# Optimization experiments

Measured on AMD Instinct MI355X. Metric: run time of the kernel, lower is better.

Reference implementation:

```python
import jax, jax.numpy as jnp
import numpy as np

N_USERS = 50000
N_ENTITIES = 250000
N_RELATIONS = 24
EMBED_DIM = 128
RELATION_DIM = 128
KG_BATCH = 16384
KG_L2_LAMBDA = 1e-5


def _l2_loss_mean(x):
    # mean over batch of (||x||^2 / 2)
    return jnp.mean(jnp.sum(x * x, axis=1) / 2.0)


def setup_inputs() -> dict:
    key = jax.random.key(0)
    k1, k2, k3, k4, k5, k6, k7 = jax.random.split(key, 7)
    n_total = N_ENTITIES + N_USERS
    # xavier-uniform-like init scale
    s_e = float(np.sqrt(6.0 / (n_total + EMBED_DIM)))
    s_r = float(np.sqrt(6.0 / (N_RELATIONS + RELATION_DIM)))
    s_m = float(np.sqrt(6.0 / (EMBED_DIM + RELATION_DIM)))
    entity_user_embed = jax.random.uniform(k1, (n_total, EMBED_DIM), jnp.float32, -s_e, s_e)
    relation_embed = jax.random.uniform(k2, (N_RELATIONS, RELATION_DIM), jnp.float32, -s_r, s_r)
    trans_M = jax.random.uniform(k3, (N_RELATIONS, EMBED_DIM, RELATION_DIM), jnp.float32, -s_m, s_m)
    h = jax.random.randint(k4, (KG_BATCH,), 0, n_total, dtype=jnp.int64 if jax.config.jax_enable_x64 else jnp.int32)
    r = jax.random.randint(k5, (KG_BATCH,), 0, N_RELATIONS, dtype=h.dtype)
    pos_t = jax.random.randint(k6, (KG_BATCH,), 0, n_total, dtype=h.dtype)
    neg_t = jax.random.randint(k7, (KG_BATCH,), 0, n_total, dtype=h.dtype)
    return {
        "entity_user_embed": entity_user_embed,
        "relation_embed": relation_embed,
        "trans_M": trans_M,
        "h": h,
        "r": r,
        "pos_t": pos_t,
        "neg_t": neg_t,
    }


def reference(entity_user_embed, relation_embed, trans_M, h, r, pos_t, neg_t):
    # KGAT.calc_kg_loss (mode='train_kg')
    r_embed = relation_embed[r]            # [B, R]
    W_r = trans_M[r]                       # [B, E, R] per-edge TransR matrix (gather)
    h_embed = entity_user_embed[h]         # [B, E]
    pos_t_embed = entity_user_embed[pos_t] # [B, E]
    neg_t_embed = entity_user_embed[neg_t] # [B, E]

    # bmm([B,1,E], [B,E,R]) -> [B,R]
    r_mul_h = jnp.einsum('be,ber->br', h_embed, W_r)
    r_mul_pos_t = jnp.einsum('be,ber->br', pos_t_embed, W_r)
    r_mul_neg_t = jnp.einsum('be,ber->br', neg_t_embed, W_r)

    pos_score = jnp.sum(jnp.square(r_mul_h + r_embed - r_mul_pos_t), axis=1)
    neg_score = jnp.sum(jnp.square(r_mul_h + r_embed - r_mul_neg_t), axis=1)

    kg_loss = jnp.mean(-jax.nn.log_sigmoid(neg_score - pos_score))
    l2_loss = (_l2_loss_mean(r_mul_h) + _l2_loss_mean(r_embed)
               + _l2_loss_mean(r_mul_pos_t) + _l2_loss_mean(r_mul_neg_t))
    return kg_loss + KG_L2_LAMBDA * l2_loss
```

## Files before the change

kernel.cpp:

```cpp
#include <hip/hip_runtime.h>
#include <math.h>

#define KG_B    16384
#define KG_D    128
#define KG_NR   24
#define KG_TM   32
#define KG_BPAD (KG_B + KG_NR * KG_TM)
#define KG_NGRP (KG_BPAD / KG_TM)

#define WS_BSUM KG_BPAD
#define WS_PREW_BYTES 131072

typedef __attribute__((ext_vector_type(8))) short bf16x8;
typedef __attribute__((ext_vector_type(4))) float f32x4;

__device__ __forceinline__ unsigned bf16r(float f) {
    return (__float_as_uint(f) + 0x8000u) >> 16;
}
__device__ __forceinline__ unsigned pack2(float lo, float hi) {
    return bf16r(lo) | (bf16r(hi) << 16);
}

__global__ __launch_bounds__(1024) void kg_sort_prep(const int* __restrict__ r,
                                                     const float* __restrict__ M,
                                                     int* __restrict__ perm,
                                                     unsigned short* __restrict__ preW) {
    __shared__ int cntw[16][25];
    __shared__ int basew[16][25];
    __shared__ int pbase_s[24];
    __shared__ int cnt_tot[24];
    __shared__ int total_s;
    __shared__ __align__(16) unsigned short sWp[KG_D * KG_D];

    const int t = threadIdx.x;

    if (blockIdx.x != 0) {
        const int k  = blockIdx.x - 1;
        const int e  = t >> 3;
        const int c0 = (t & 7) * 16;
        const float* src = M + ((size_t)k << 14) + (size_t)e * KG_D + c0;
        float4 rw[4];
#pragma unroll
        for (int f = 0; f < 4; ++f) rw[f] = ((const float4*)src)[f];
#pragma unroll
        for (int dc = 0; dc < 16; ++dc) {
            const int col = c0 + dc;
            const float v = ((const float*)&rw[0])[dc];
            sWp[col * KG_D + (e ^ ((col & 7) << 3))] = (unsigned short)bf16r(v);
        }
        __syncthreads();
        uint4* dst = (uint4*)(preW + ((size_t)k << 14));
        const uint4* s4 = (const uint4*)sWp;
        dst[2 * t]     = s4[2 * t];
        dst[2 * t + 1] = s4[2 * t + 1];
        return;
    }

    const int w = t >> 6;
    int* cz = &cntw[0][0];
    for (int i = t; i < 16 * 25; i += 1024) cz[i] = 0;
    __syncthreads();

    int kt[16];
#pragma unroll
    for (int j = 0; j < 16; ++j) kt[j] = r[j * 1024 + t];
#pragma unroll
    for (int j = 0; j < 16; ++j) atomicAdd(&cntw[w][kt[j]], 1);
    __syncthreads();

    if (t < 24) {
        int s = 0;
        for (int w2 = 0; w2 < 16; ++w2) { basew[w2][t] = s; s += cntw[w2][t]; }
        cnt_tot[t] = s;
    }
    __syncthreads();
    if (t == 0) {
        int run = 0;
        for (int k = 0; k < 24; ++k) {
            pbase_s[k] = run;
            run += (cnt_tot[k] + (KG_TM - 1)) & ~(KG_TM - 1);
        }
        total_s = run;
    }
    __syncthreads();
    if (t < 24)
        for (int w2 = 0; w2 < 16; ++w2) basew[w2][t] += pbase_s[t];
    for (int i = t; i < 16 * 25; i += 1024) cz[i] = 0;
    __syncthreads();

#pragma unroll
    for (int j = 0; j < 16; ++j) {
        const int k = kt[j];
        const int pos = basew[w][k] + atomicAdd(&cntw[w][k], 1);
        perm[pos] = j * 1024 + t;
    }
    __syncthreads();

    if (t < 24) {
        const int e0 = pbase_s[t] + cnt_tot[t];
        const int e1 = pbase_s[t] + ((cnt_tot[t] + (KG_TM - 1)) & ~(KG_TM - 1));
        for (int p = e0; p < e1; ++p) perm[p] = -1;
    }
    for (int i = total_s + t; i < KG_BPAD; i += 1024) perm[i] = -1;
}

__global__ __launch_bounds__(256, 2) void kg_main(
    const float* __restrict__ ent, const float* __restrict__ rel,
    const unsigned short* __restrict__ preW,
    const int* __restrict__ h,     const int* __restrict__ r,
    const int* __restrict__ pt,    const int* __restrict__ nt,
    const int* __restrict__ perm,  float* __restrict__ bsum)
{
    __shared__ __align__(16) unsigned short sX[3 * KG_TM * KG_D];
    __shared__ __align__(16) unsigned short sW[KG_D * KG_D];
    __shared__ float sScr[2][KG_TM][4];

    const int tid   = threadIdx.x;
    const int slot0 = blockIdx.x * KG_TM;
    const int p0    = perm[slot0];
    if (p0 < 0) {
        if (tid == 0) bsum[blockIdx.x] = 0.f;
        return;
    }
    const int rb = __builtin_amdgcn_readfirstlane(r[p0]);

    {
        const char* gsrc = (const char*)(preW + ((size_t)rb << 14));
        char* ldsb = (char*)&sW[0];
        const int w4   = tid >> 6;
        const int lane = tid & 63;
#pragma unroll
        for (int q = 0; q < 8; ++q) {
            const int off = q * 4096 + w4 * 1024;
            __builtin_amdgcn_global_load_lds(
                (const unsigned int*)(gsrc + off + lane * 16),
                (unsigned int*)(ldsb + off), 16, 0, 0);
        }
    }

    {
        const int g  = tid >> 3;
        const int e0 = (tid & 7) * 16;
        const int pg = perm[slot0 + g];
        const int bb = pg < 0 ? p0 : pg;
        const int idx3[3] = { h[bb], pt[bb], nt[bb] };
        const int sw = (g & 7) << 3;
#pragma unroll
        for (int t3 = 0; t3 < 3; ++t3) {
            const float* src = ent + (size_t)idx3[t3] * KG_D + e0;
            const float4 f0 = ((const float4*)src)[0];
            const float4 f1 = ((const float4*)src)[1];
            const float4 f2 = ((const float4*)src)[2];
            const float4 f3 = ((const float4*)src)[3];
            uint4 u0, u1;
            u0.x = pack2(f0.x, f0.y); u0.y = pack2(f0.z, f0.w);
            u0.z = pack2(f1.x, f1.y); u0.w = pack2(f1.z, f1.w);
            u1.x = pack2(f2.x, f2.y); u1.y = pack2(f2.z, f2.w);
            u1.z = pack2(f3.x, f3.y); u1.w = pack2(f3.z, f3.w);
            unsigned short* base = sX + t3 * (KG_TM * KG_D) + g * KG_D;
            *(uint4*)(base + ((e0    ) ^ sw)) = u0;
            *(uint4*)(base + ((e0 + 8) ^ sw)) = u1;
        }
    }
    __syncthreads();

    const int l   = tid & 63;
    const int w   = tid >> 6;
    const int rt  = w & 1;
    const int chs = w >> 1;
    const int li  = l & 15;
    const int kq  = l >> 4;

    const int ar  = rt * 16 + li;
    const int asw = (ar & 7) << 3;

    f32x4 acc[3][4];
#pragma unroll
    for (int t3 = 0; t3 < 3; ++t3)
#pragma unroll
        for (int n = 0; n < 4; ++n) acc[t3][n] = (f32x4)0.f;

#pragma unroll
    for (int kk = 0; kk < 4; ++kk) {
        const int e0 = kk * 32 + kq * 8;
        bf16x8 af[3];
#pragma unroll
        for (int t3 = 0; t3 < 3; ++t3)
            af[t3] = *(const bf16x8*)&sX[t3 * (KG_TM * KG_D) + ar * KG_D + (e0 ^ asw)];
#pragma unroll
        for (int n = 0; n < 4; ++n) {
            const int col = chs * 64 + n * 16 + li;
            const bf16x8 bfr = *(const bf16x8*)&sW[col * KG_D + (e0 ^ ((col & 7) << 3))];
            acc[0][n] = __builtin_amdgcn_mfma_f32_16x16x32_bf16(af[0], bfr, acc[0][n], 0, 0, 0);
            acc[1][n] = __builtin_amdgcn_mfma_f32_16x16x32_bf16(af[1], bfr, acc[1][n], 0, 0, 0);
            acc[2][n] = __builtin_amdgcn_mfma_f32_16x16x32_bf16(af[2], bfr, acc[2][n], 0, 0, 0);
        }
    }

    float ps[4] = {0,0,0,0}, ns[4] = {0,0,0,0}, sq[4] = {0,0,0,0};
    const float* relrow = rel + (size_t)rb * KG_D + chs * 64;
#pragma unroll
    for (int n = 0; n < 4; ++n) {
        const float rv = relrow[n * 16 + li];
#pragma unroll
        for (int j = 0; j < 4; ++j) {
            const float va = acc[0][n][j];
            const float vp = acc[1][n][j];
            const float vn = acc[2][n][j];
            const float s  = va + rv;
            const float dp = s - vp;
            const float dn = s - vn;
            ps[j] += dp * dp;
            ns[j] += dn * dn;
            sq[j] += va * va + vp * vp + vn * vn + rv * rv;
        }
    }
#pragma unroll
    for (int j = 0; j < 4; ++j)
#pragma unroll
        for (int m = 1; m < 16; m <<= 1) {
            ps[j] += __shfl_xor(ps[j], m);
            ns[j] += __shfl_xor(ns[j], m);
            sq[j] += __shfl_xor(sq[j], m);
        }

    if (li == 0) {
#pragma unroll
        for (int j = 0; j < 4; ++j) {
            const int row = rt * 16 + kq * 4 + j;
            sScr[chs][row][0] = ps[j];
            sScr[chs][row][1] = ns[j];
            sScr[chs][row][2] = sq[j];
        }
    }
    __syncthreads();

    if (tid < 64) {
        float term = 0.f;
        if (tid < KG_TM) {
            const int row = tid;
            const float P = sScr[0][row][0] + sScr[1][row][0];
            const float N = sScr[0][row][1] + sScr[1][row][1];
            const float S = sScr[0][row][2] + sScr[1][row][2];
            const int pg = perm[slot0 + row];
            if (pg >= 0) {
                const float x = P - N;
                term = fmaxf(x, 0.f) + log1pf(expf(-fabsf(x)))
                     + 5e-6f * S;
            }
        }
#pragma unroll
        for (int off = 16; off > 0; off >>= 1) term += __shfl_down(term, off);
        if (tid == 0) bsum[blockIdx.x] = term;
    }
}

__global__ __launch_bounds__(256) void kg_final(const float* __restrict__ bsum,
                                                float* __restrict__ out) {
    __shared__ float s[256];
    const int t = threadIdx.x;
    float acc = 0.f;
    for (int i = t; i < KG_NGRP; i += 256) acc += bsum[i];
    s[t] = acc;
    __syncthreads();
    for (int off = 128; off > 0; off >>= 1) {
        if (t < off) s[t] += s[t + off];
        __syncthreads();
    }
    if (t == 0) out[0] = s[0] * (1.0f / (float)KG_B);
}

extern "C" void kernel_launch(void* const* d_in, const int* in_sizes, int n_in,
                              void* d_out, int out_size, void* d_ws, size_t ws_size,
                              hipStream_t stream) {
    const float* ent = (const float*)d_in[0];
    const float* rel = (const float*)d_in[1];
    const float* M   = (const float*)d_in[2];
    const int*   h   = (const int*)d_in[3];
    const int*   r   = (const int*)d_in[4];
    const int*   pt  = (const int*)d_in[5];
    const int*   nt  = (const int*)d_in[6];

    int*            perm = (int*)d_ws;
    float*          bsum = (float*)d_ws + WS_BSUM;
    unsigned short* preW = (unsigned short*)((char*)d_ws + WS_PREW_BYTES);
    float*          out  = (float*)d_out;

    kg_sort_prep<<<1 + KG_NR, 1024, 0, stream>>>(r, M, perm, preW);
    kg_main     <<<KG_NGRP, 256, 0, stream>>>(ent, rel, preW, h, r, pt, nt, perm, bsum);
    kg_final    <<<1, 256, 0, stream>>>(bsum, out);
}
```

Baseline: 27.89 us.

## Load A-fragments directly to registers and fuse final reduction via atomics

Removes the shared-memory staging of gathered entity rows: each lane now loads and converts its MFMA A-fragments straight from global memory into registers. This frees LDS, so launch bounds are raised to 3 blocks per CU. It also drops the separate final-reduction kernel. Each block instead adds its partial sum into a fixed-point 64-bit global accumulator, and the last block to finish writes the result. The trade-offs are uncoalesced-ish per-lane gathers, global atomic contention, and fixed-point quantization of the sum.

```diff
diff --git a/kernel.cpp b/kernel.cpp
--- a/kernel.cpp
+++ b/kernel.cpp
@@ -8,8 +8,10 @@
 #define KG_BPAD (KG_B + KG_NR * KG_TM)
 #define KG_NGRP (KG_BPAD / KG_TM)
 
-#define WS_BSUM KG_BPAD
+#define WS_ACC_BYTES  68608
+#define WS_DONE_BYTES 68616
 #define WS_PREW_BYTES 131072
+#define KG_SCALE      1099511627776.0
 
 typedef __attribute__((ext_vector_type(8))) short bf16x8;
 typedef __attribute__((ext_vector_type(4))) float f32x4;
@@ -24,6 +26,8 @@
 __global__ __launch_bounds__(1024) void kg_sort_prep(const int* __restrict__ r,
                                                      const float* __restrict__ M,
                                                      int* __restrict__ perm,
+                                                     unsigned long long* __restrict__ acc,
+                                                     unsigned int* __restrict__ done,
                                                      unsigned short* __restrict__ preW) {
     __shared__ int cntw[16][25];
     __shared__ int basew[16][25];
@@ -56,6 +60,8 @@
         return;
     }
 
+    if (t == 0) { *acc = 0ull; *done = 0u; }
+
     const int w = t >> 6;
     int* cz = &cntw[0][0];
     for (int i = t; i < 16 * 25; i += 1024) cz[i] = 0;
@@ -104,170 +110,156 @@
     for (int i = total_s + t; i < KG_BPAD; i += 1024) perm[i] = -1;
 }
 
-__global__ __launch_bounds__(256, 2) void kg_main(
+__global__ __launch_bounds__(256, 3) void kg_main(
     const float* __restrict__ ent, const float* __restrict__ rel,
     const unsigned short* __restrict__ preW,
     const int* __restrict__ h,     const int* __restrict__ r,
     const int* __restrict__ pt,    const int* __restrict__ nt,
-    const int* __restrict__ perm,  float* __restrict__ bsum)
+    const int* __restrict__ perm,
+    unsigned long long* __restrict__ acc,
+    unsigned int* __restrict__ done,
+    float* __restrict__ out)
 {
-    __shared__ __align__(16) unsigned short sX[3 * KG_TM * KG_D];
     __shared__ __align__(16) unsigned short sW[KG_D * KG_D];
     __shared__ float sScr[2][KG_TM][4];
 
     const int tid   = threadIdx.x;
     const int slot0 = blockIdx.x * KG_TM;
     const int p0    = perm[slot0];
-    if (p0 < 0) {
-        if (tid == 0) bsum[blockIdx.x] = 0.f;
-        return;
-    }
-    const int rb = __builtin_amdgcn_readfirstlane(r[p0]);
-
-    {
-        const char* gsrc = (const char*)(preW + ((size_t)rb << 14));
-        char* ldsb = (char*)&sW[0];
-        const int w4   = tid >> 6;
-        const int lane = tid & 63;
-#pragma unroll
-        for (int q = 0; q < 8; ++q) {
-            const int off = q * 4096 + w4 * 1024;
-            __builtin_amdgcn_global_load_lds(
-                (const unsigned int*)(gsrc + off + lane * 16),
-                (unsigned int*)(ldsb + off), 16, 0, 0);
-        }
-    }
-
-    {
-        const int g  = tid >> 3;
-        const int e0 = (tid & 7) * 16;
-        const int pg = perm[slot0 + g];
-        const int bb = pg < 0 ? p0 : pg;
+
+    float bs = 0.f;
+
+    if (p0 >= 0) {
+        const int rb = __builtin_amdgcn_readfirstlane(r[p0]);
+
+        {
+            const char* gsrc = (const char*)(preW + ((size_t)rb << 14));
+            char* ldsb = (char*)&sW[0];
+            const int w4   = tid >> 6;
+            const int lane = tid & 63;
+#pragma unroll
+            for (int q = 0; q < 8; ++q) {
+                const int off = q * 4096 + w4 * 1024;
+                __builtin_amdgcn_global_load_lds(
+                    (const unsigned int*)(gsrc + off + lane * 16),
+                    (unsigned int*)(ldsb + off), 16, 0, 0);
+            }
+        }
+
+        const int l   = tid & 63;
+        const int w   = tid >> 6;
+        const int rt  = w & 1;
+        const int chs = w >> 1;
+        const int li  = l & 15;
+        const int kq  = l >> 4;
+
+        const int ar = rt * 16 + li;
+        const int pr = perm[slot0 + ar];
+        const int bb = pr < 0 ? p0 : pr;
         const int idx3[3] = { h[bb], pt[bb], nt[bb] };
-        const int sw = (g & 7) << 3;
+        bf16x8 af[3][4];
 #pragma unroll
         for (int t3 = 0; t3 < 3; ++t3) {
-            const float* src = ent + (size_t)idx3[t3] * KG_D + e0;
-            const float4 f0 = ((const float4*)src)[0];
-            const float4 f1 = ((const float4*)src)[1];
-            const float4 f2 = ((const float4*)src)[2];
-            const float4 f3 = ((const float4*)src)[3];
-            uint4 u0, u1;
-            u0.x = pack2(f0.x, f0.y); u0.y = pack2(f0.z, f0.w);
-            u0.z = pack2(f1.x, f1.y); u0.w = pack2(f1.z, f1.w);
-            u1.x = pack2(f2.x, f2.y); u1.y = pack2(f2.z, f2.w);
-            u1.z = pack2(f3.x, f3.y); u1.w = pack2(f3.z, f3.w);
-            unsigned short* base = sX + t3 * (KG_TM * KG_D) + g * KG_D;
-            *(uint4*)(base + ((e0    ) ^ sw)) = u0;
-            *(uint4*)(base + ((e0 + 8) ^ sw)) = u1;
-        }
-    }
-    __syncthreads();
-
-    const int l   = tid & 63;
-    const int w   = tid >> 6;
-    const int rt  = w & 1;
-    const int chs = w >> 1;
-    const int li  = l & 15;
-    const int kq  = l >> 4;
-
-    const int ar  = rt * 16 + li;
-    const int asw = (ar & 7) << 3;
-
-    f32x4 acc[3][4];
-#pragma unroll
-    for (int t3 = 0; t3 < 3; ++t3)
-#pragma unroll
-        for (int n = 0; n < 4; ++n) acc[t3][n] = (f32x4)0.f;
-
-#pragma unroll
-    for (int kk = 0; kk < 4; ++kk) {
-        const int e0 = kk * 32 + kq * 8;
-        bf16x8 af[3];
+            const float* xb = ent + (size_t)idx3[t3] * KG_D;
+#pragma unroll
+            for (int kk = 0; kk < 4; ++kk) {
+                const int e0 = kk * 32 + kq * 8;
+                const float4 a0 = *(const float4*)(xb + e0);
+                const float4 a1 = *(const float4*)(xb + e0 + 4);
+                union { uint4 u; bf16x8 v; } cv;
+                cv.u.x = pack2(a0.x, a0.y); cv.u.y = pack2(a0.z, a0.w);
+                cv.u.z = pack2(a1.x, a1.y); cv.u.w = pack2(a1.z, a1.w);
+                af[t3][kk] = cv.v;
+            }
+        }
+        __syncthreads();
+
+        f32x4 accf[3][4];
 #pragma unroll
         for (int t3 = 0; t3 < 3; ++t3)
-            af[t3] = *(const bf16x8*)&sX[t3 * (KG_TM * KG_D) + ar * KG_D + (e0 ^ asw)];
+#pragma unroll
+            for (int n = 0; n < 4; ++n) accf[t3][n] = (f32x4)0.f;
+
+#pragma unroll
+        for (int kk = 0; kk < 4; ++kk) {
+            const int e0 = kk * 32 + kq * 8;
+#pragma unroll
+            for (int n = 0; n < 4; ++n) {
+                const int col = chs * 64 + n * 16 + li;
+                const bf16x8 bfr = *(const bf16x8*)&sW[col * KG_D + (e0 ^ ((col & 7) << 3))];
+                accf[0][n] = __builtin_amdgcn_mfma_f32_16x16x32_bf16(af[0][kk], bfr, accf[0][n], 0, 0, 0);
+                accf[1][n] = __builtin_amdgcn_mfma_f32_16x16x32_bf16(af[1][kk], bfr, accf[1][n], 0, 0, 0);
+                accf[2][n] = __builtin_amdgcn_mfma_f32_16x16x32_bf16(af[2][kk], bfr, accf[2][n], 0, 0, 0);
+            }
+        }
+
+        float ps[4] = {0,0,0,0}, ns[4] = {0,0,0,0}, sq[4] = {0,0,0,0};
+        const float* relrow = rel + (size_t)rb * KG_D + chs * 64;
 #pragma unroll
         for (int n = 0; n < 4; ++n) {
-            const int col = chs * 64 + n * 16 + li;
-            const bf16x8 bfr = *(const bf16x8*)&sW[col * KG_D + (e0 ^ ((col & 7) << 3))];
-            acc[0][n] = __builtin_amdgcn_mfma_f32_16x16x32_bf16(af[0], bfr, acc[0][n], 0, 0, 0);
-            acc[1][n] = __builtin_amdgcn_mfma_f32_16x16x32_bf16(af[1], bfr, acc[1][n], 0, 0, 0);
-            acc[2][n] = __builtin_amdgcn_mfma_f32_16x16x32_bf16(af[2], bfr, acc[2][n], 0, 0, 0);
-        }
-    }
-
-    float ps[4] = {0,0,0,0}, ns[4] = {0,0,0,0}, sq[4] = {0,0,0,0};
-    const float* relrow = rel + (size_t)rb * KG_D + chs * 64;
-#pragma unroll
-    for (int n = 0; n < 4; ++n) {
-        const float rv = relrow[n * 16 + li];
-#pragma unroll
-        for (int j = 0; j < 4; ++j) {
-            const float va = acc[0][n][j];
-            const float vp = acc[1][n][j];
-            const float vn = acc[2][n][j];
-            const float s  = va + rv;
-            const float dp = s - vp;
-            const float dn = s - vn;
-            ps[j] += dp * dp;
-            ns[j] += dn * dn;
-            sq[j] += va * va + vp * vp + vn * vn + rv * rv;
-        }
-    }
-#pragma unroll
-    for (int j = 0; j < 4; ++j)
-#pragma unroll
-        for (int m = 1; m < 16; m <<= 1) {
-            ps[j] += __shfl_xor(ps[j], m);
-            ns[j] += __shfl_xor(ns[j], m);
-            sq[j] += __shfl_xor(sq[j], m);
-        }
-
-    if (li == 0) {
-#pragma unroll
-        for (int j = 0; j < 4; ++j) {
-            const int row = rt * 16 + kq * 4 + j;
-            sScr[chs][row][0] = ps[j];
-            sScr[chs][row][1] = ns[j];
-            sScr[chs][row][2] = sq[j];
-        }
-    }
-    __syncthreads();
-
-    if (tid < 64) {
-        float term = 0.f;
-        if (tid < KG_TM) {
-            const int row = tid;
-            const float P = sScr[0][row][0] + sScr[1][row][0];
-            const float N = sScr[0][row][1] + sScr[1][row][1];
-            const float S = sScr[0][row][2] + sScr[1][row][2];
-            const int pg = perm[slot0 + row];
-            if (pg >= 0) {
-                const float x = P - N;
-                term = fmaxf(x, 0.f) + log1pf(expf(-fabsf(x)))
-                     + 5e-6f * S;
-            }
-        }
-#pragma unroll
-        for (int off = 16; off > 0; off >>= 1) term += __shfl_down(term, off);
-        if (tid == 0) bsum[blockIdx.x] = term;
-    }
-}
-
-__global__ __launch_bounds__(256) void kg_final(const float* __restrict__ bsum,
-                                                float* __restrict__ out) {
-    __shared__ float s[256];
-    const int t = threadIdx.x;
-    float acc = 0.f;
-    for (int i = t; i < KG_NGRP; i += 256) acc += bsum[i];
-    s[t] = acc;
-    __syncthreads();
-    for (int off = 128; off > 0; off >>= 1) {
-        if (t < off) s[t] += s[t + off];
+            const float rv = relrow[n * 16 + li];
+#pragma unroll
+            for (int j = 0; j < 4; ++j) {
+                const float va = accf[0][n][j];
+                const float vp = accf[1][n][j];
+                const float vn = accf[2][n][j];
+                const float s  = va + rv;
+                const float dp = s - vp;
+                const float dn = s - vn;
+                ps[j] += dp * dp;
+                ns[j] += dn * dn;
+                sq[j] += va * va + vp * vp + vn * vn + rv * rv;
+            }
+        }
+#pragma unroll
+        for (int j = 0; j < 4; ++j)
+#pragma unroll
+            for (int m = 1; m < 16; m <<= 1) {
+                ps[j] += __shfl_xor(ps[j], m);
+                ns[j] += __shfl_xor(ns[j], m);
+                sq[j] += __shfl_xor(sq[j], m);
+            }
+
+        if (li == 0) {
+#pragma unroll
+            for (int j = 0; j < 4; ++j) {
+                const int row = rt * 16 + kq * 4 + j;
+                sScr[chs][row][0] = ps[j];
+                sScr[chs][row][1] = ns[j];
+                sScr[chs][row][2] = sq[j];
+            }
+        }
         __syncthreads();
-    }
-    if (t == 0) out[0] = s[0] * (1.0f / (float)KG_B);
+
+        if (tid < 64) {
+            float term = 0.f;
+            if (tid < KG_TM) {
+                const int row = tid;
+                const float P = sScr[0][row][0] + sScr[1][row][0];
+                const float N = sScr[0][row][1] + sScr[1][row][1];
+                const float S = sScr[0][row][2] + sScr[1][row][2];
+                const int pg = perm[slot0 + row];
+                if (pg >= 0) {
+                    const float x = P - N;
+                    term = fmaxf(x, 0.f) + log1pf(expf(-fabsf(x)))
+                         + 5e-6f * S;
+                }
+            }
+#pragma unroll
+            for (int off = 16; off > 0; off >>= 1) term += __shfl_down(term, off);
+            bs = term;
+        }
+    }
+
+    if (tid == 0) {
+        if (bs > 0.f)
+            atomicAdd(acc, (unsigned long long)__double2ll_rn((double)bs * KG_SCALE));
+        __threadfence();
+        if (atomicAdd(done, 1u) == (unsigned)(KG_NGRP - 1)) {
+            const unsigned long long tot = atomicAdd(acc, 0ull);
+            out[0] = (float)((double)tot * (1.0 / KG_SCALE) * (1.0 / (double)KG_B));
+        }
+    }
 }
 
 extern "C" void kernel_launch(void* const* d_in, const int* in_sizes, int n_in,
@@ -281,12 +273,13 @@
     const int*   pt  = (const int*)d_in[5];
     const int*   nt  = (const int*)d_in[6];
 
-    int*            perm = (int*)d_ws;
-    float*          bsum = (float*)d_ws + WS_BSUM;
-    unsigned short* preW = (unsigned short*)((char*)d_ws + WS_PREW_BYTES);
-    float*          out  = (float*)d_out;
-
-    kg_sort_prep<<<1 + KG_NR, 1024, 0, stream>>>(r, M, perm, preW);
-    kg_main     <<<KG_NGRP, 256, 0, stream>>>(ent, rel, preW, h, r, pt, nt, perm, bsum);
-    kg_final    <<<1, 256, 0, stream>>>(bsum, out);
-}
+    int*                perm = (int*)d_ws;
+    unsigned long long* acc  = (unsigned long long*)((char*)d_ws + WS_ACC_BYTES);
+    unsigned int*       done = (unsigned int*)((char*)d_ws + WS_DONE_BYTES);
+    unsigned short*     preW = (unsigned short*)((char*)d_ws + WS_PREW_BYTES);
+    float*              out  = (float*)d_out;
+
+    kg_sort_prep<<<1 + KG_NR, 1024, 0, stream>>>(r, M, perm, acc, done, preW);
+    kg_main     <<<KG_NGRP, 256, 0, stream>>>(ent, rel, preW, h, r, pt, nt, perm,
+                                              acc, done, out);
+}
```

Measured after the change: 37.79 us. +35.5%, slower.
